# Kernel optimization log

Hardware: AMD Instinct MI355X
Metric: run time of the kernel (lower is better)

The kernel has to match this reference:

```python
import jax, jax.numpy as jnp
import numpy as np

C = 512
GROUPS = 32
EPS = 1e-6


def group_norm(x, gamma, beta):
    b, c, h, w = x.shape
    xg = x.reshape(b, GROUPS, c // GROUPS, h, w)
    mu = xg.mean(axis=(2, 3, 4), keepdims=True)
    var = xg.var(axis=(2, 3, 4), keepdims=True)
    xn = (xg - mu) * jax.lax.rsqrt(var + EPS)
    xn = xn.reshape(b, c, h, w)
    return xn * gamma[None, :, None, None] + beta[None, :, None, None]


def conv1x1(x, w, b):
    # x: [b,c,h,w], w: [out,in], b: [out]
    return jnp.einsum('bchw,oc->bohw', x, w) + b[None, :, None, None]


def setup_inputs() -> dict:
    key = jax.random.key(0)
    ks = jax.random.split(key, 12)
    s = 1.0 / np.sqrt(C)
    return {
        'x': jax.random.normal(ks[0], (2, C, 64, 64), dtype=jnp.float32),
        'gn_gamma': jnp.ones((C,), jnp.float32),
        'gn_beta': jnp.zeros((C,), jnp.float32),
        'wq': jax.random.normal(ks[1], (C, C), jnp.float32) * s,
        'bq': jax.random.normal(ks[2], (C,), jnp.float32) * 0.01,
        'wk': jax.random.normal(ks[3], (C, C), jnp.float32) * s,
        'bk': jax.random.normal(ks[4], (C,), jnp.float32) * 0.01,
        'wv': jax.random.normal(ks[5], (C, C), jnp.float32) * s,
        'bv': jax.random.normal(ks[6], (C,), jnp.float32) * 0.01,
        'wo': jax.random.normal(ks[7], (C, C), jnp.float32) * s,
        'bo': jax.random.normal(ks[8], (C,), jnp.float32) * 0.01,
    }


def reference(x, gn_gamma, gn_beta, wq, bq, wk, bk, wv, bv, wo, bo):
    b, c, h, w = x.shape
    hn = group_norm(x, gn_gamma, gn_beta)
    q = conv1x1(hn, wq, bq).reshape(b, c, h * w)  # [b,c,n]
    k = conv1x1(hn, wk, bk).reshape(b, c, h * w)
    v = conv1x1(hn, wv, bv).reshape(b, c, h * w)
    scale = c ** (-0.5)
    # scores[b,i,j] = q[:, :, i] . k[:, :, j]
    scores = jnp.einsum('bci,bcj->bij', q, k) * scale
    attn = jax.nn.softmax(scores, axis=2)
    # out[b,c,i] = sum_j v[b,c,j] * attn[b,i,j]
    out = jnp.einsum('bcj,bij->bci', v, attn).reshape(b, c, h, w)
    out = conv1x1(out, wo, bo)
    return x + out
```

## Files before the change

kernel.cpp:

```cpp
#include <hip/hip_runtime.h>
#include <cstdint>
#include <cstddef>

typedef __bf16 bf16;
typedef __bf16 bf16x8 __attribute__((ext_vector_type(8)));
typedef float f32x4 __attribute__((ext_vector_type(4)));

static constexpr int Cdim = 512;
static constexpr int Ndim = 4096;
static constexpr size_t NCe = (size_t)Ndim * Cdim;
static constexpr size_t QKVs = (size_t)Ndim * 1536;
static constexpr size_t Ss = (size_t)Ndim * Ndim;

#define AS1 __attribute__((address_space(1)))
#define AS3 __attribute__((address_space(3)))

__device__ __forceinline__ void async16(bf16* lds, const bf16* g) {
  __builtin_amdgcn_global_load_lds((AS1 void*)(g), (AS3 void*)(lds), 16, 0, 0);
}

__global__ __launch_bounds__(256) void prep(const float* __restrict__ wq, const float* __restrict__ wk,
                                            const float* __restrict__ wv, const float* __restrict__ wo,
                                            const float* __restrict__ bq, const float* __restrict__ bk,
                                            const float* __restrict__ bv,
                                            bf16* __restrict__ wqkv, bf16* __restrict__ wob,
                                            float* __restrict__ bqkv) {
  int i = blockIdx.x * 256 + threadIdx.x;
  if (i < 262144) wqkv[i] = (bf16)wq[i];
  else if (i < 524288) wqkv[i] = (bf16)wk[i - 262144];
  else if (i < 786432) wqkv[i] = (bf16)wv[i - 524288];
  else if (i < 1048576) wob[i - 786432] = (bf16)wo[i - 786432];
  else if (i < 1048576 + 1536) {
    int j = i - 1048576;
    bqkv[j] = j < 512 ? bq[j] : j < 1024 ? bk[j - 512] : bv[j - 1024];
  }
}

__global__ __launch_bounds__(256) void gn_stats(const float* __restrict__ x, float* __restrict__ stats) {
  const int bg = blockIdx.x;
  const float4* base = (const float4*)(x + (size_t)bg * 65536);
  float s = 0.f, q = 0.f;
  for (int i = threadIdx.x; i < 16384; i += 256) {
    float4 v = base[i];
    s += v.x + v.y + v.z + v.w;
    q += v.x * v.x + v.y * v.y + v.z * v.z + v.w * v.w;
  }
#pragma unroll
  for (int off = 32; off > 0; off >>= 1) { s += __shfl_xor(s, off); q += __shfl_xor(q, off); }
  __shared__ float rs[4], rq[4];
  const int lane = threadIdx.x & 63, wave = threadIdx.x >> 6;
  if (lane == 0) { rs[wave] = s; rq[wave] = q; }
  __syncthreads();
  if (threadIdx.x == 0) {
    float st = rs[0] + rs[1] + rs[2] + rs[3];
    float qt = rq[0] + rq[1] + rq[2] + rq[3];
    float mean = st * (1.f / 65536.f);
    float var = qt * (1.f / 65536.f) - mean * mean;
    stats[2 * bg] = mean;
    stats[2 * bg + 1] = rsqrtf(var + 1e-6f);
  }
}

__global__ __launch_bounds__(256) void gn_norm_t(const float* __restrict__ x, const float* __restrict__ stats,
                                                 const float* __restrict__ gamma, const float* __restrict__ beta,
                                                 bf16* __restrict__ hn_t) {
  const int n0 = blockIdx.x * 64, c0 = blockIdx.y * 64, b = blockIdx.z;
  const float* xb = x + (size_t)b * NCe;
  __shared__ float tile[64][65];
  const int t = threadIdx.x;
  const int tx = t & 15, ty = t >> 4;
#pragma unroll
  for (int i = 0; i < 4; ++i) {
    int c = ty * 4 + i;
    float4 v = *(const float4*)&xb[(size_t)(c0 + c) * Ndim + n0 + tx * 4];
    tile[c][tx * 4 + 0] = v.x; tile[c][tx * 4 + 1] = v.y;
    tile[c][tx * 4 + 2] = v.z; tile[c][tx * 4 + 3] = v.w;
  }
  __syncthreads();
  const int c8 = t & 7, nr = t >> 3;
#pragma unroll
  for (int i = 0; i < 2; ++i) {
    int nl = nr + i * 32;
    bf16x8 o;
#pragma unroll
    for (int j = 0; j < 8; ++j) {
      int cl = c8 * 8 + j;
      int c = c0 + cl;
      int g = b * 32 + (c >> 4);
      float mean = stats[2 * g], rstd = stats[2 * g + 1];
      float v = (tile[cl][nl] - mean) * rstd * gamma[c] + beta[c];
      o[j] = (bf16)v;
    }
    *(bf16x8*)&hn_t[((size_t)b * Ndim + n0 + nl) * Cdim + c0 + c8 * 8] = o;
  }
}

template <int BMT, int BNT, int EPI, int SPLITK>
__global__ __launch_bounds__(256) void gemm_bt(const bf16* __restrict__ A, size_t lda, size_t asb,
                                               const bf16* __restrict__ B, size_t ldb, size_t bsb,
                                               void* __restrict__ Cp, size_t csb,
                                               int M, int N, int K,
                                               const float* __restrict__ bias, float scale,
                                               const float* __restrict__ resid, size_t rsb,
                                               int nx, int nxy, int sgy, int sgx) {
  const int P = gridDim.x >> 3;
  const int f = (blockIdx.x & 7) * P + (blockIdx.x >> 3);
  const int z = f / nxy;
  const int r = f - z * nxy;
  const int stw = sgy * sgx;
  const int st = r / stw, w = r - st * stw;
  const int nsx = nx / sgx;
  const int sy = st / nsx, sx = st - sy * nsx;
  const int wy = w / sgx;
  const int by = sy * sgy + wy;
  const int bx = sx * sgx + (w - wy * sgx);

  constexpr int MI = BMT / 32, NI = BNT / 32;
  const int zb = z / SPLITK, sk = z - zb * SPLITK;
  A += (size_t)zb * asb;
  B += (size_t)zb * bsb;
  if constexpr (EPI == 4) resid += (size_t)zb * rsb;
  const size_t cofs = (size_t)zb * csb;
  const int kspan = K / SPLITK;
  const int kbeg = sk * kspan, kend = kbeg + kspan;
  const int m0 = by * BMT, n0 = bx * BNT;
  __shared__ bf16 As[2][BMT * 32];
  __shared__ bf16 Bs[2][BNT * 32];
  const int tid = threadIdx.x;
  const int lane = tid & 63, wave = tid >> 6;
  const bf16* gA = A + (size_t)(m0 + (tid >> 2)) * lda + (tid & 3) * 8;
  const bf16* gB = B + (size_t)(n0 + (tid >> 2)) * ldb + (tid & 3) * 8;
  const int wm = (wave & 1) * (BMT / 2), wn = (wave >> 1) * (BNT / 2);
  const int lrow = lane & 15, koff = (lane >> 4) * 8;
  f32x4 acc[MI][NI];
#pragma unroll
  for (int mi = 0; mi < MI; ++mi)
#pragma unroll
    for (int ni = 0; ni < NI; ++ni) acc[mi][ni] = (f32x4){0.f, 0.f, 0.f, 0.f};

  auto stage = [&](int buf, int k0) {
    bf16* lA = As[buf] + tid * 8;
    bf16* lB = Bs[buf] + tid * 8;
#pragma unroll
    for (int it = 0; it < BMT / 64; ++it) async16(lA + it * 2048, gA + (size_t)it * 64 * lda + k0);
#pragma unroll
    for (int it = 0; it < BNT / 64; ++it) async16(lB + it * 2048, gB + (size_t)it * 64 * ldb + k0);
  };

  stage(0, kbeg);
  int buf = 0;
  for (int k0 = kbeg; k0 < kend; k0 += 32) {
    __syncthreads();
    if (k0 + 32 < kend) stage(buf ^ 1, k0 + 32);
    const bf16* fA = As[buf] + (wm + lrow) * 32 + koff;
    const bf16* fB = Bs[buf] + (wn + lrow) * 32 + koff;
    bf16x8 af[MI], bfr[NI];
#pragma unroll
    for (int mi = 0; mi < MI; ++mi) af[mi] = *(const bf16x8*)(fA + mi * 512);
#pragma unroll
    for (int ni = 0; ni < NI; ++ni) bfr[ni] = *(const bf16x8*)(fB + ni * 512);
#pragma unroll
    for (int mi = 0; mi < MI; ++mi)
#pragma unroll
      for (int ni = 0; ni < NI; ++ni)
        acc[mi][ni] = __builtin_amdgcn_mfma_f32_16x16x32_bf16(af[mi], bfr[ni], acc[mi][ni], 0, 0, 0);
    buf ^= 1;
  }

  const int col = lane & 15, rb = (lane >> 4) * 4;
#pragma unroll
  for (int mi = 0; mi < MI; ++mi) {
#pragma unroll
    for (int ni = 0; ni < NI; ++ni) {
      const int gn = n0 + wn + ni * 16 + col;
      const int gm0 = m0 + wm + mi * 16 + rb;
#pragma unroll
      for (int r2 = 0; r2 < 4; ++r2) {
        const int gm = gm0 + r2;
        const size_t ci = cofs + (size_t)gm * N + gn;
        float vv = acc[mi][ni][r2];
        if constexpr (EPI == 0) ((bf16*)Cp)[ci] = (bf16)(vv + bias[gn]);
        else if constexpr (EPI == 2) ((bf16*)Cp)[ci] = (bf16)(vv * scale);
        else if constexpr (EPI == 3) ((bf16*)Cp)[ci] = (bf16)vv;
        else if constexpr (EPI == 4) {
          if (SPLITK == 1 || sk == 0) vv += bias[gm] + resid[(size_t)gm * N + gn];
          atomicAdd(&((float*)Cp)[ci], vv);
        }
      }
    }
  }
}

__global__ __launch_bounds__(256) void softmax_rows(bf16* __restrict__ S, size_t bstride) {
  const int t = threadIdx.x;
  bf16* p = S + (size_t)blockIdx.y * bstride + (size_t)blockIdx.x * 4096 + t * 16;
  bf16x8 a = *(const bf16x8*)p;
  bf16x8 c = *(const bf16x8*)(p + 8);
  float f[16];
#pragma unroll
  for (int j = 0; j < 8; ++j) { f[j] = (float)a[j]; f[8 + j] = (float)c[j]; }
  float m = f[0];
#pragma unroll
  for (int j = 1; j < 16; ++j) m = fmaxf(m, f[j]);
#pragma unroll
  for (int off = 32; off > 0; off >>= 1) m = fmaxf(m, __shfl_xor(m, off));
  __shared__ float wm_[4], ws_[4];
  const int lane = t & 63, wave = t >> 6;
  if (lane == 0) wm_[wave] = m;
  __syncthreads();
  m = fmaxf(fmaxf(wm_[0], wm_[1]), fmaxf(wm_[2], wm_[3]));
  float s = 0.f;
#pragma unroll
  for (int j = 0; j < 16; ++j) { f[j] = __expf(f[j] - m); s += f[j]; }
#pragma unroll
  for (int off = 32; off > 0; off >>= 1) s += __shfl_xor(s, off);
  if (lane == 0) ws_[wave] = s;
  __syncthreads();
  s = ws_[0] + ws_[1] + ws_[2] + ws_[3];
  const float r = 1.f / s;
#pragma unroll
  for (int j = 0; j < 8; ++j) { a[j] = (bf16)(f[j] * r); c[j] = (bf16)(f[8 + j] * r); }
  *(bf16x8*)p = a;
  *(bf16x8*)(p + 8) = c;
}

extern "C" void kernel_launch(void* const* d_in, const int* in_sizes, int n_in,
                              void* d_out, int out_size, void* d_ws, size_t ws_size,
                              hipStream_t stream) {
  (void)in_sizes; (void)n_in; (void)out_size;
  const float* x     = (const float*)d_in[0];
  const float* gamma = (const float*)d_in[1];
  const float* beta  = (const float*)d_in[2];
  const float* wq = (const float*)d_in[3];
  const float* bq = (const float*)d_in[4];
  const float* wk = (const float*)d_in[5];
  const float* bk = (const float*)d_in[6];
  const float* wv = (const float*)d_in[7];
  const float* bv = (const float*)d_in[8];
  const float* wo = (const float*)d_in[9];
  const float* bo = (const float*)d_in[10];
  float* out = (float*)d_out;

  char* ws = (char*)d_ws;
  size_t off = 0;
  auto alloc = [&](size_t bytes) {
    void* p = ws + off;
    off += (bytes + 1023) & ~(size_t)1023;
    return p;
  };
  bf16* wqkv  = (bf16*)alloc(786432 * 2);
  bf16* wob   = (bf16*)alloc(262144 * 2);
  float* bqkv = (float*)alloc(1536 * 4);
  float* stats = (float*)alloc(64 * 2 * 4);
  bf16* hn_t  = (bf16*)alloc(NCe * 2 * 2);
  bf16* qkv_t = (bf16*)alloc(QKVs * 2 * 2);
  bf16* vo    = (bf16*)alloc(NCe * 2 * 2);
  const bool two = (off + 2 * Ss * 2) <= ws_size;
  bf16* S = (bf16*)alloc((two ? 2 * Ss : Ss) * 2);

  hipMemsetAsync(out, 0, 2 * NCe * sizeof(float), stream);
  prep<<<4102, 256, 0, stream>>>(wq, wk, wv, wo, bq, bk, bv, wqkv, wob, bqkv);
  gn_stats<<<64, 256, 0, stream>>>(x, stats);
  gn_norm_t<<<dim3(64, 8, 2), 256, 0, stream>>>(x, stats, gamma, beta, hn_t);

  const float scale = 0.044194173824159216f;

  gemm_bt<128, 128, 0, 1><<<768, 256, 0, stream>>>(
      hn_t, 512, NCe, wqkv, 512, 0, qkv_t, QKVs, Ndim, 1536, Cdim, bqkv, 1.f, nullptr, 0,
      12, 384, 8, 12);
  gemm_bt<64, 128, 3, 1><<<512, 256, 0, stream>>>(
      wob, 512, 0, qkv_t + 1024, 1536, QKVs, vo, NCe, Cdim, Ndim, Cdim, nullptr, 1.f, nullptr, 0,
      32, 256, 8, 8);

  if (two) {
    gemm_bt<128, 128, 2, 1><<<2048, 256, 0, stream>>>(
        qkv_t, 1536, QKVs, qkv_t + 512, 1536, QKVs, S, Ss, Ndim, Ndim, Cdim, nullptr, scale, nullptr, 0,
        32, 1024, 16, 16);
    softmax_rows<<<dim3(4096, 2), 256, 0, stream>>>(S, Ss);
    gemm_bt<128, 128, 4, 4><<<1024, 256, 0, stream>>>(
        vo, 4096, NCe, S, 4096, Ss, out, NCe, Cdim, Ndim, Ndim, bo, 1.f, x, NCe,
        32, 128, 4, 1);
  } else {
    for (int b = 0; b < 2; ++b) {
      gemm_bt<128, 128, 2, 1><<<1024, 256, 0, stream>>>(
          qkv_t + b * QKVs, 1536, 0, qkv_t + b * QKVs + 512, 1536, 0, S, 0,
          Ndim, Ndim, Cdim, nullptr, scale, nullptr, 0,
          32, 1024, 16, 16);
      softmax_rows<<<dim3(4096, 1), 256, 0, stream>>>(S, 0);
      gemm_bt<128, 128, 4, 4><<<512, 256, 0, stream>>>(
          vo + b * NCe, 4096, 0, S, 4096, 0, out + b * NCe, 0,
          Cdim, Ndim, Ndim, bo, 1.f, x + b * NCe, 0,
          32, 128, 4, 1);
    }
  }
}
```

Measured before the change: 350.5 us.

## Load GEMM fragments directly from global memory, dropping LDS staging

The GEMM kernel no longer stages A/B tiles through double-buffered LDS with async global-to-LDS loads and per-iteration barriers. Each lane now reads its MFMA fragments straight from global memory through per-row pointers, the k-loop is unrolled by 2, and launch bounds request 2 blocks per CU. This removes LDS traffic and __syncthreads, but it loses cross-wave data sharing, so each wave re-reads A and B rows from global or L2. The strided 16-byte reads may also coalesce poorly.

```diff
diff --git a/kernel.cpp b/kernel.cpp
--- a/kernel.cpp
+++ b/kernel.cpp
@@ -11,13 +11,6 @@
 static constexpr size_t NCe = (size_t)Ndim * Cdim;
 static constexpr size_t QKVs = (size_t)Ndim * 1536;
 static constexpr size_t Ss = (size_t)Ndim * Ndim;
-
-#define AS1 __attribute__((address_space(1)))
-#define AS3 __attribute__((address_space(3)))
-
-__device__ __forceinline__ void async16(bf16* lds, const bf16* g) {
-  __builtin_amdgcn_global_load_lds((AS1 void*)(g), (AS3 void*)(lds), 16, 0, 0);
-}
 
 __global__ __launch_bounds__(256) void prep(const float* __restrict__ wq, const float* __restrict__ wk,
                                             const float* __restrict__ wv, const float* __restrict__ wo,
@@ -96,13 +89,13 @@
 }
 
 template <int BMT, int BNT, int EPI, int SPLITK>
-__global__ __launch_bounds__(256) void gemm_bt(const bf16* __restrict__ A, size_t lda, size_t asb,
-                                               const bf16* __restrict__ B, size_t ldb, size_t bsb,
-                                               void* __restrict__ Cp, size_t csb,
-                                               int M, int N, int K,
-                                               const float* __restrict__ bias, float scale,
-                                               const float* __restrict__ resid, size_t rsb,
-                                               int nx, int nxy, int sgy, int sgx) {
+__global__ __launch_bounds__(256, 2) void gemm_bt(const bf16* __restrict__ A, size_t lda, size_t asb,
+                                                  const bf16* __restrict__ B, size_t ldb, size_t bsb,
+                                                  void* __restrict__ Cp, size_t csb,
+                                                  int M, int N, int K,
+                                                  const float* __restrict__ bias, float scale,
+                                                  const float* __restrict__ resid, size_t rsb,
+                                                  int nx, int nxy, int sgy, int sgx) {
   const int P = gridDim.x >> 3;
   const int f = (blockIdx.x & 7) * P + (blockIdx.x >> 3);
   const int z = f / nxy;
@@ -122,49 +115,41 @@
   if constexpr (EPI == 4) resid += (size_t)zb * rsb;
   const size_t cofs = (size_t)zb * csb;
   const int kspan = K / SPLITK;
-  const int kbeg = sk * kspan, kend = kbeg + kspan;
+  const int kbeg = sk * kspan;
   const int m0 = by * BMT, n0 = bx * BNT;
-  __shared__ bf16 As[2][BMT * 32];
-  __shared__ bf16 Bs[2][BNT * 32];
   const int tid = threadIdx.x;
   const int lane = tid & 63, wave = tid >> 6;
-  const bf16* gA = A + (size_t)(m0 + (tid >> 2)) * lda + (tid & 3) * 8;
-  const bf16* gB = B + (size_t)(n0 + (tid >> 2)) * ldb + (tid & 3) * 8;
   const int wm = (wave & 1) * (BMT / 2), wn = (wave >> 1) * (BNT / 2);
   const int lrow = lane & 15, koff = (lane >> 4) * 8;
+
+  const bf16* pa[MI];
+  const bf16* pb[NI];
+#pragma unroll
+  for (int mi = 0; mi < MI; ++mi)
+    pa[mi] = A + (size_t)(m0 + wm + mi * 16 + lrow) * lda + kbeg + koff;
+#pragma unroll
+  for (int ni = 0; ni < NI; ++ni)
+    pb[ni] = B + (size_t)(n0 + wn + ni * 16 + lrow) * ldb + kbeg + koff;
+
   f32x4 acc[MI][NI];
 #pragma unroll
   for (int mi = 0; mi < MI; ++mi)
 #pragma unroll
     for (int ni = 0; ni < NI; ++ni) acc[mi][ni] = (f32x4){0.f, 0.f, 0.f, 0.f};
 
-  auto stage = [&](int buf, int k0) {
-    bf16* lA = As[buf] + tid * 8;
-    bf16* lB = Bs[buf] + tid * 8;
-#pragma unroll
-    for (int it = 0; it < BMT / 64; ++it) async16(lA + it * 2048, gA + (size_t)it * 64 * lda + k0);
-#pragma unroll
-    for (int it = 0; it < BNT / 64; ++it) async16(lB + it * 2048, gB + (size_t)it * 64 * ldb + k0);
-  };
-
-  stage(0, kbeg);
-  int buf = 0;
-  for (int k0 = kbeg; k0 < kend; k0 += 32) {
-    __syncthreads();
-    if (k0 + 32 < kend) stage(buf ^ 1, k0 + 32);
-    const bf16* fA = As[buf] + (wm + lrow) * 32 + koff;
-    const bf16* fB = Bs[buf] + (wn + lrow) * 32 + koff;
+  const int iters = kspan / 32;
+#pragma unroll 2
+  for (int it = 0; it < iters; ++it) {
     bf16x8 af[MI], bfr[NI];
 #pragma unroll
-    for (int mi = 0; mi < MI; ++mi) af[mi] = *(const bf16x8*)(fA + mi * 512);
-#pragma unroll
-    for (int ni = 0; ni < NI; ++ni) bfr[ni] = *(const bf16x8*)(fB + ni * 512);
+    for (int mi = 0; mi < MI; ++mi) { af[mi] = *(const bf16x8*)pa[mi]; pa[mi] += 32; }
+#pragma unroll
+    for (int ni = 0; ni < NI; ++ni) { bfr[ni] = *(const bf16x8*)pb[ni]; pb[ni] += 32; }
 #pragma unroll
     for (int mi = 0; mi < MI; ++mi)
 #pragma unroll
       for (int ni = 0; ni < NI; ++ni)
         acc[mi][ni] = __builtin_amdgcn_mfma_f32_16x16x32_bf16(af[mi], bfr[ni], acc[mi][ni], 0, 0, 0);
-    buf ^= 1;
   }
 
   const int col = lane & 15, rb = (lane >> 4) * 4;
```

After: 512.9 us. 1.46x slower.
